# Kernel optimization log

Hardware: AMD Instinct MI355X
Metric: run time of the kernel (lower is better)

The kernel has to match this reference:

```python
import jax, jax.numpy as jnp
import numpy as np
from jax import lax

B, T, D, H = 128, 512, 512, 512
FORGET_BIAS = 1.0  # TF BasicLSTMCell default


def setup_inputs() -> dict:
    key = jax.random.key(0)
    k1, k2, k3 = jax.random.split(key, 3)
    scale = 1.0 / np.sqrt(D + H)
    return {
        "word_vectors": jax.random.normal(k1, (B, T, D), dtype=jnp.float32),
        "num_words": jax.random.randint(k2, (B,), 0, T, dtype=jnp.int32),
        "init_c": jnp.zeros((B, H), dtype=jnp.float32),
        "init_h": jnp.zeros((B, H), dtype=jnp.float32),
        "W": jax.random.normal(k3, (D + H, 4 * H), dtype=jnp.float32) * scale,  # gates i,j,f,o
        "b": jnp.zeros((4 * H,), dtype=jnp.float32),
    }


def reference(word_vectors, num_words, init_c, init_h, W, b):
    # word_vectors: [B, T, D] -> time-major [T, B, D]
    xs = jnp.transpose(word_vectors, (1, 0, 2))
    ts = jnp.arange(T, dtype=num_words.dtype)

    def step(carry, inp):
        c, h = carry
        x, t = inp
        z = jnp.concatenate([x, h], axis=-1) @ W + b  # [B, 4H]
        i, j, f, o = jnp.split(z, 4, axis=-1)  # TF gate order
        new_c = c * jax.nn.sigmoid(f + FORGET_BIAS) + jax.nn.sigmoid(i) * jnp.tanh(j)
        new_h = jnp.tanh(new_c) * jax.nn.sigmoid(o)
        mask = (t < num_words)[:, None]  # [B, 1]
        # static_rnn sequence_length semantics: copy state through, zero outputs
        c2 = jnp.where(mask, new_c, c)
        h2 = jnp.where(mask, new_h, h)
        out = jnp.where(mask, new_h, jnp.zeros_like(new_h))
        return (c2, h2), out

    (final_c, final_h), outputs = lax.scan(step, (init_c, init_h), (xs, ts))
    # outputs: [T, B, H] (time-major, like the list returned by static_rnn)
    return outputs, final_c, final_h
```

## Files before the change

### kernel.cpp

```cpp
#include <hip/hip_runtime.h>


#define B_ 128
#define T_ 512
#define D_ 512
#define H_ 512
#define POISON 0xFFFFFFFFu

typedef __bf16 bf16x8 __attribute__((ext_vector_type(8)));
typedef float f32x4 __attribute__((ext_vector_type(4)));
typedef unsigned long long u64;

static __device__ __forceinline__ unsigned short f2bf(float f) {
  return __builtin_bit_cast(unsigned short, (__bf16)f);
}
static __device__ __forceinline__ float fast_sigmoid(float x) {
  return __builtin_amdgcn_rcpf(1.f + __expf(-x));
}
static __device__ __forceinline__ float fast_tanh(float x) {
  float xc = fminf(fmaxf(x, -15.f), 15.f);
  float t = __expf(-2.f * xc);
  return (1.f - t) * __builtin_amdgcn_rcpf(1.f + t);
}
static __device__ __forceinline__ bool clean64(u64 v) {
  return ((unsigned int)v != POISON) && ((unsigned int)(v >> 32) != POISON);
}

#define LBAR()                                             \
  do {                                                     \
    __asm__ volatile("s_waitcnt lgkmcnt(0)" ::: "memory"); \
    __builtin_amdgcn_s_barrier();                          \
    __asm__ volatile("" ::: "memory");                     \
  } while (0)

__global__ __launch_bounds__(256) void pack_w_kernel(const float* __restrict__ W,
                                                     unsigned short* __restrict__ Wp) {
  int tid = blockIdx.x * 256 + threadIdx.x;
  int j = tid & 7;
  int lane = (tid >> 3) & 63;
  int f = tid >> 9;
  int kt = f & 31;
  int w = (f >> 5) & 7;
  int hb = f >> 8;
  int k = (kt << 5) + ((lane >> 4) << 3) + j;
  int col = ((w & 3) << 9) + (hb << 5) + ((w >> 2) << 4) + (lane & 15);
  Wp[tid] = f2bf(W[k * 2048 + col]);
}

__global__ __launch_bounds__(1024) void init_poison_kernel(unsigned int* __restrict__ hg) {
  hg[blockIdx.x * 1024 + threadIdx.x] = POISON;
}

__global__ __launch_bounds__(512, 2) void lstm_persistent(
    const float* __restrict__ wv, const int* __restrict__ nw,
    const float* __restrict__ ic, const float* __restrict__ ih,
    const float* __restrict__ bias, const unsigned short* __restrict__ Wp,
    unsigned int* __restrict__ hg, float* __restrict__ out) {
  __shared__ __align__(16) unsigned short hlds[16 * 512];
  __shared__ __align__(16) unsigned short xlds[2][16 * 512];
  __shared__ float zbuf[8][16][17];

  const int tid = threadIdx.x;
  const int wgid = blockIdx.x;
  const int mg = wgid & 7;
  const int hb = wgid >> 3;
  const int w = tid >> 6;
  const int lane = tid & 63;
  const int g = w & 3;
  const int jj = w >> 2;

  const int er = tid >> 5;
  const int ec = tid & 31;
  const int grow = (mg << 4) + er;
  const int gcol = (hb << 5) + ec;

  const int nwv = nw[grow];
  float c_reg = ic[grow * H_ + gcol];
  float h_reg = ih[grow * H_ + gcol];

  uint4 wfrag[32];
  {
    const uint4* wp = (const uint4*)Wp + (size_t)((hb * 8 + w) * 32) * 64 + lane;
#pragma unroll
    for (int kt = 0; kt < 32; ++kt) wfrag[kt] = wp[kt * 64];
  }
  const float bv = bias[(g << 9) + (hb << 5) + (jj << 4) + (lane & 15)];

  auto slotp = [&](int s) { return hg + (size_t)(s * 8 + mg) * 4096; };

  const int hslot = (hb << 9) + ((er | ((ec >> 3) << 4)) << 3) + (ec & 7);

  auto publish_h = [&](unsigned int* dst) {
    unsigned int hv = (unsigned int)f2bf(h_reg);
    unsigned int up = (unsigned int)__shfl_down((int)hv, 1);
    if ((tid & 1) == 0)
      __hip_atomic_store(dst + (hslot >> 1), hv | (up << 16), __ATOMIC_RELAXED,
                         __HIP_MEMORY_SCOPE_AGENT);
  };

  auto wait_stage = [&](const unsigned int* slot) {
    const u64* s = (const u64*)slot;
    const u64* cs0 = s + ((2 * w) << 7);
    const u64* cs1 = s + ((2 * w + 1) << 7);
    u64 a0, a1, b0, b1;
    while (true) {
      a0 = __hip_atomic_load(cs0 + lane, __ATOMIC_RELAXED, __HIP_MEMORY_SCOPE_AGENT);
      a1 = __hip_atomic_load(cs0 + 64 + lane, __ATOMIC_RELAXED, __HIP_MEMORY_SCOPE_AGENT);
      b0 = __hip_atomic_load(cs1 + lane, __ATOMIC_RELAXED, __HIP_MEMORY_SCOPE_AGENT);
      b1 = __hip_atomic_load(cs1 + 64 + lane, __ATOMIC_RELAXED, __HIP_MEMORY_SCOPE_AGENT);
      bool ok = clean64(a0) && clean64(a1) && clean64(b0) && clean64(b1);
      if (__all(ok)) break;
      __builtin_amdgcn_s_sleep(1);
    }
    u64* d = (u64*)hlds;
    d[((2 * w) << 7) + lane] = a0;
    d[((2 * w) << 7) + 64 + lane] = a1;
    d[((2 * w + 1) << 7) + lane] = b0;
    d[((2 * w + 1) << 7) + 64 + lane] = b1;
  };

  auto repoison = [&](unsigned int* slot) {
    if (tid < 256)
      __hip_atomic_store(slot + (hb << 8) + tid, POISON, __ATOMIC_RELAXED,
                         __HIP_MEMORY_SCOPE_AGENT);
  };

  float4 xr[4];
  auto xissue = [&](int tt) {
    if (tt >= T_) return;
#pragma unroll
    for (int s2 = 0; s2 < 2; ++s2) {
      int e = tid + (s2 << 9);
      int ktx = e >> 6;
      int le = e & 63;
      int r = le & 15;
      int d = (ktx << 5) + ((le >> 4) << 3);
      const float* src = wv + ((size_t)((mg << 4) + r) * T_ + tt) * D_ + d;
      xr[2 * s2] = *(const float4*)src;
      xr[2 * s2 + 1] = *(const float4*)(src + 4);
    }
  };
  auto xcommit = [&](int buf, int tt) {
    if (tt >= T_) return;
#pragma unroll
    for (int s2 = 0; s2 < 2; ++s2) {
      int e = tid + (s2 << 9);
      int ktx = e >> 6;
      int le = e & 63;
      float4 xa = xr[2 * s2], xb = xr[2 * s2 + 1];
      bf16x8 v;
      v[0] = (__bf16)xa.x; v[1] = (__bf16)xa.y; v[2] = (__bf16)xa.z; v[3] = (__bf16)xa.w;
      v[4] = (__bf16)xb.x; v[5] = (__bf16)xb.y; v[6] = (__bf16)xb.z; v[7] = (__bf16)xb.w;
      *(bf16x8*)&xlds[buf][(ktx << 9) + (le << 3)] = v;
    }
  };

  auto xpart = [&](int buf) {
    f32x4 a = {0.f, 0.f, 0.f, 0.f};
#pragma unroll
    for (int kt = 0; kt < 16; ++kt) {
      bf16x8 af = *(const bf16x8*)&xlds[buf][(kt << 9) + (lane << 3)];
      a = __builtin_amdgcn_mfma_f32_16x16x32_bf16(
          af, __builtin_bit_cast(bf16x8, wfrag[kt]), a, 0, 0, 0);
    }
    return a;
  };

  xissue(0); xcommit(0, 0);
  xissue(1); xcommit(1, 1);
#pragma unroll
  for (int s2 = 0; s2 < 2; ++s2) {
    int e = tid + (s2 << 9);
    int ktx = e >> 6;
    int le = e & 63;
    int r = le & 15;
    int d = (ktx << 5) + ((le >> 4) << 3);
    const float* src = ih + (size_t)((mg << 4) + r) * H_ + d;
    float4 ha = *(const float4*)src;
    float4 hbv = *(const float4*)(src + 4);
    bf16x8 v;
    v[0] = (__bf16)ha.x; v[1] = (__bf16)ha.y; v[2] = (__bf16)ha.z; v[3] = (__bf16)ha.w;
    v[4] = (__bf16)hbv.x; v[5] = (__bf16)hbv.y; v[6] = (__bf16)hbv.z; v[7] = (__bf16)hbv.w;
    *(bf16x8*)&hlds[(ktx << 9) + (le << 3)] = v;
  }
  __syncthreads();
  f32x4 acc = xpart(0);

  for (int t = 0; t < T_; ++t) {
    const int par = t & 1;
    unsigned int* hdst = slotp((t + 1) % 3);

    xissue(t + 2);

    f32x4 acc2 = {0.f, 0.f, 0.f, 0.f};
#pragma unroll
    for (int kt = 0; kt < 8; ++kt) {
      bf16x8 a0 = *(const bf16x8*)&hlds[((2 * kt) << 9) + (lane << 3)];
      bf16x8 a1 = *(const bf16x8*)&hlds[((2 * kt + 1) << 9) + (lane << 3)];
      acc = __builtin_amdgcn_mfma_f32_16x16x32_bf16(
          a0, __builtin_bit_cast(bf16x8, wfrag[16 + 2 * kt]), acc, 0, 0, 0);
      acc2 = __builtin_amdgcn_mfma_f32_16x16x32_bf16(
          a1, __builtin_bit_cast(bf16x8, wfrag[17 + 2 * kt]), acc2, 0, 0, 0);
    }
    {
      int q = lane >> 4, cl = lane & 15;
#pragma unroll
      for (int v = 0; v < 4; ++v)
        zbuf[w][q * 4 + v][cl] = acc[v] + acc2[v] + bv;
    }
    LBAR();
    {
      int ej = ec >> 4, ecl = ec & 15;
      float zi = zbuf[ej * 4 + 0][er][ecl];
      float zj = zbuf[ej * 4 + 1][er][ecl];
      float zf = zbuf[ej * 4 + 2][er][ecl];
      float zo = zbuf[ej * 4 + 3][er][ecl];
      float si = fast_sigmoid(zi);
      float sf = fast_sigmoid(zf + 1.f);
      float so = fast_sigmoid(zo);
      float tj = fast_tanh(zj);
      float nc = c_reg * sf + si * tj;
      float nh = fast_tanh(nc) * so;
      bool m = t < nwv;
      c_reg = m ? nc : c_reg;
      h_reg = m ? nh : h_reg;
      publish_h(hdst);
      out[(size_t)t * (B_ * H_) + grow * H_ + gcol] = m ? nh : 0.f;
    }
    LBAR();

    if (t + 1 < T_) {
      acc = xpart(1 - par);
      wait_stage(hdst);
      repoison(slotp(t % 3));
      xcommit(par, t + 2);
    }
    __syncthreads();
  }

  size_t base = (size_t)T_ * (B_ * H_);
  out[base + grow * H_ + gcol] = c_reg;
  out[base + B_ * H_ + grow * H_ + gcol] = h_reg;
}

extern "C" void kernel_launch(void* const* d_in, const int* in_sizes, int n_in,
                              void* d_out, int out_size, void* d_ws, size_t ws_size,
                              hipStream_t stream) {
  const float* wv = (const float*)d_in[0];
  const int* nw = (const int*)d_in[1];
  const float* ic = (const float*)d_in[2];
  const float* ih = (const float*)d_in[3];
  const float* W = (const float*)d_in[4];
  const float* bias = (const float*)d_in[5];
  float* out = (float*)d_out;

  char* ws = (char*)d_ws;
  unsigned short* Wp = (unsigned short*)ws;
  unsigned int* hg = (unsigned int*)(ws + (4u << 20));

  init_poison_kernel<<<96, 1024, 0, stream>>>(hg);
  pack_w_kernel<<<(1 << 21) / 256, 256, 0, stream>>>(W, Wp);
  lstm_persistent<<<128, 512, 0, stream>>>(wv, nw, ic, ih, bias, Wp, hg, out);
}
```

Baseline: 1.655 ms.

## Widen h-exchange ring to 8 slots, trim barriers, split MFMA accumulator chains

The recurrent h exchange buffer grows from a 3-slot ring to an 8-slot ring, and the workspace init kernel is enlarged to cover it. The post-publish workgroup barrier is dropped, and a full __syncthreads is used only every fourth step. The wait loop spins without sleeping for its first few polls and gives up after a fixed cap. The x and h MFMA reductions are split into two and four independent accumulator chains to shorten dependency latency. The aim is to cut per-timestep barrier and polling latency on the serial critical path. The poll cap can silently proceed with stale or poisoned data if a producer is slow.

```diff
diff --git a/kernel.cpp b/kernel.cpp
--- a/kernel.cpp
+++ b/kernel.cpp
@@ -6,6 +6,7 @@
 #define D_ 512
 #define H_ 512
 #define POISON 0xFFFFFFFFu
+#define POLL_CAP 8192
 
 typedef __bf16 bf16x8 __attribute__((ext_vector_type(8)));
 typedef float f32x4 __attribute__((ext_vector_type(4)));
@@ -47,7 +48,7 @@
   Wp[tid] = f2bf(W[k * 2048 + col]);
 }
 
-__global__ __launch_bounds__(1024) void init_poison_kernel(unsigned int* __restrict__ hg) {
+__global__ __launch_bounds__(1024) void init_ws_kernel(unsigned int* __restrict__ hg) {
   hg[blockIdx.x * 1024 + threadIdx.x] = POISON;
 }
 
@@ -100,17 +101,20 @@
 
   auto wait_stage = [&](const unsigned int* slot) {
     const u64* s = (const u64*)slot;
-    const u64* cs0 = s + ((2 * w) << 7);
-    const u64* cs1 = s + ((2 * w + 1) << 7);
+    const u64* p0 = s + ((2 * w) << 7) + lane;
+    const u64* p1 = p0 + 64;
+    const u64* p2 = s + ((2 * w + 1) << 7) + lane;
+    const u64* p3 = p2 + 64;
     u64 a0, a1, b0, b1;
+    int it = 0;
     while (true) {
-      a0 = __hip_atomic_load(cs0 + lane, __ATOMIC_RELAXED, __HIP_MEMORY_SCOPE_AGENT);
-      a1 = __hip_atomic_load(cs0 + 64 + lane, __ATOMIC_RELAXED, __HIP_MEMORY_SCOPE_AGENT);
-      b0 = __hip_atomic_load(cs1 + lane, __ATOMIC_RELAXED, __HIP_MEMORY_SCOPE_AGENT);
-      b1 = __hip_atomic_load(cs1 + 64 + lane, __ATOMIC_RELAXED, __HIP_MEMORY_SCOPE_AGENT);
-      bool ok = clean64(a0) && clean64(a1) && clean64(b0) && clean64(b1);
-      if (__all(ok)) break;
-      __builtin_amdgcn_s_sleep(1);
+      a0 = __hip_atomic_load(p0, __ATOMIC_RELAXED, __HIP_MEMORY_SCOPE_AGENT);
+      a1 = __hip_atomic_load(p1, __ATOMIC_RELAXED, __HIP_MEMORY_SCOPE_AGENT);
+      b0 = __hip_atomic_load(p2, __ATOMIC_RELAXED, __HIP_MEMORY_SCOPE_AGENT);
+      b1 = __hip_atomic_load(p3, __ATOMIC_RELAXED, __HIP_MEMORY_SCOPE_AGENT);
+      if (__all(clean64(a0) && clean64(a1) && clean64(b0) && clean64(b1))) break;
+      if (++it > POLL_CAP) break;
+      if (it > 8) __builtin_amdgcn_s_sleep(1);
     }
     u64* d = (u64*)hlds;
     d[((2 * w) << 7) + lane] = a0;
@@ -155,15 +159,21 @@
     }
   };
 
+  f32x4 xA, xB;
   auto xpart = [&](int buf) {
-    f32x4 a = {0.f, 0.f, 0.f, 0.f};
-#pragma unroll
-    for (int kt = 0; kt < 16; ++kt) {
-      bf16x8 af = *(const bf16x8*)&xlds[buf][(kt << 9) + (lane << 3)];
-      a = __builtin_amdgcn_mfma_f32_16x16x32_bf16(
-          af, __builtin_bit_cast(bf16x8, wfrag[kt]), a, 0, 0, 0);
-    }
-    return a;
+    f32x4 A = {0.f, 0.f, 0.f, 0.f};
+    f32x4 Bc = {0.f, 0.f, 0.f, 0.f};
+#pragma unroll
+    for (int kt = 0; kt < 8; ++kt) {
+      bf16x8 a0 = *(const bf16x8*)&xlds[buf][(kt << 9) + (lane << 3)];
+      bf16x8 a1 = *(const bf16x8*)&xlds[buf][((kt + 8) << 9) + (lane << 3)];
+      A = __builtin_amdgcn_mfma_f32_16x16x32_bf16(
+          a0, __builtin_bit_cast(bf16x8, wfrag[kt]), A, 0, 0, 0);
+      Bc = __builtin_amdgcn_mfma_f32_16x16x32_bf16(
+          a1, __builtin_bit_cast(bf16x8, wfrag[kt + 8]), Bc, 0, 0, 0);
+    }
+    xA = A;
+    xB = Bc;
   };
 
   xissue(0); xcommit(0, 0);
@@ -184,29 +194,35 @@
     *(bf16x8*)&hlds[(ktx << 9) + (le << 3)] = v;
   }
   __syncthreads();
-  f32x4 acc = xpart(0);
+  xpart(0);
 
   for (int t = 0; t < T_; ++t) {
     const int par = t & 1;
-    unsigned int* hdst = slotp((t + 1) % 3);
-
-    xissue(t + 2);
-
-    f32x4 acc2 = {0.f, 0.f, 0.f, 0.f};
-#pragma unroll
-    for (int kt = 0; kt < 8; ++kt) {
-      bf16x8 a0 = *(const bf16x8*)&hlds[((2 * kt) << 9) + (lane << 3)];
-      bf16x8 a1 = *(const bf16x8*)&hlds[((2 * kt + 1) << 9) + (lane << 3)];
-      acc = __builtin_amdgcn_mfma_f32_16x16x32_bf16(
-          a0, __builtin_bit_cast(bf16x8, wfrag[16 + 2 * kt]), acc, 0, 0, 0);
-      acc2 = __builtin_amdgcn_mfma_f32_16x16x32_bf16(
-          a1, __builtin_bit_cast(bf16x8, wfrag[17 + 2 * kt]), acc2, 0, 0, 0);
+    unsigned int* hdst = slotp((t + 1) & 7);
+
+    f32x4 c0 = xA, c1 = xB;
+    f32x4 c2 = {0.f, 0.f, 0.f, 0.f};
+    f32x4 c3 = {0.f, 0.f, 0.f, 0.f};
+#pragma unroll
+    for (int i = 0; i < 4; ++i) {
+      bf16x8 a0 = *(const bf16x8*)&hlds[((4 * i) << 9) + (lane << 3)];
+      bf16x8 a1 = *(const bf16x8*)&hlds[((4 * i + 1) << 9) + (lane << 3)];
+      bf16x8 a2 = *(const bf16x8*)&hlds[((4 * i + 2) << 9) + (lane << 3)];
+      bf16x8 a3 = *(const bf16x8*)&hlds[((4 * i + 3) << 9) + (lane << 3)];
+      c0 = __builtin_amdgcn_mfma_f32_16x16x32_bf16(
+          a0, __builtin_bit_cast(bf16x8, wfrag[16 + 4 * i]), c0, 0, 0, 0);
+      c1 = __builtin_amdgcn_mfma_f32_16x16x32_bf16(
+          a1, __builtin_bit_cast(bf16x8, wfrag[17 + 4 * i]), c1, 0, 0, 0);
+      c2 = __builtin_amdgcn_mfma_f32_16x16x32_bf16(
+          a2, __builtin_bit_cast(bf16x8, wfrag[18 + 4 * i]), c2, 0, 0, 0);
+      c3 = __builtin_amdgcn_mfma_f32_16x16x32_bf16(
+          a3, __builtin_bit_cast(bf16x8, wfrag[19 + 4 * i]), c3, 0, 0, 0);
     }
     {
       int q = lane >> 4, cl = lane & 15;
 #pragma unroll
       for (int v = 0; v < 4; ++v)
-        zbuf[w][q * 4 + v][cl] = acc[v] + acc2[v] + bv;
+        zbuf[w][q * 4 + v][cl] = (c0[v] + c1[v]) + (c2[v] + c3[v]) + bv;
     }
     LBAR();
     {
@@ -227,15 +243,16 @@
       publish_h(hdst);
       out[(size_t)t * (B_ * H_) + grow * H_ + gcol] = m ? nh : 0.f;
     }
-    LBAR();
 
     if (t + 1 < T_) {
-      acc = xpart(1 - par);
+      xissue(t + 2);
+      xpart(1 - par);
       wait_stage(hdst);
-      repoison(slotp(t % 3));
+      LBAR();
+      repoison(slotp(t & 7));
       xcommit(par, t + 2);
     }
-    __syncthreads();
+    if ((t & 3) == 3) __syncthreads(); else LBAR();
   }
 
   size_t base = (size_t)T_ * (B_ * H_);
@@ -258,7 +275,7 @@
   unsigned short* Wp = (unsigned short*)ws;
   unsigned int* hg = (unsigned int*)(ws + (4u << 20));
 
-  init_poison_kernel<<<96, 1024, 0, stream>>>(hg);
+  init_ws_kernel<<<256, 1024, 0, stream>>>(hg);
   pack_w_kernel<<<(1 << 21) / 256, 256, 0, stream>>>(W, Wp);
   lstm_persistent<<<128, 512, 0, stream>>>(wv, nw, ic, ih, bias, Wp, hg, out);
 }
```

Measured after the change: 1.517 ms. 1.09x faster.
